# Kernel tuning notes

Measured on AMD Instinct MI355X. Metric: run time of the kernel, lower is better.

Reference implementation:

```python
import jax, jax.numpy as jnp
import numpy as np

INNER_DIM = 64
HEAD_NUM = 8
D_MODEL = 512

def setup_inputs() -> dict:
    key = jax.random.key(0)
    k1, k2, k3 = jax.random.split(key, 3)
    x = jax.random.normal(k1, (4, 2048, D_MODEL), dtype=jnp.float32)
    # Keras 'uniform' initializer: U(-0.05, 0.05)
    kernel = jax.random.uniform(k2, (3 * HEAD_NUM, D_MODEL, INNER_DIM), dtype=jnp.float32, minval=-0.05, maxval=0.05)
    head_kernel = jax.random.uniform(k3, (INNER_DIM * HEAD_NUM, D_MODEL), dtype=jnp.float32, minval=-0.05, maxval=0.05)
    return {"x": x, "kernel": kernel, "head_kernel": head_kernel}

def reference(x, kernel, head_kernel):
    H, K = HEAD_NUM, INNER_DIM
    # kernel is interleaved per head: [Q0,K0,V0, Q1,K1,V1, ...]
    w = kernel.reshape(H, 3, kernel.shape[1], K)  # (H, 3, D, K)
    wq, wk, wv = w[:, 0], w[:, 1], w[:, 2]        # each (H, D, K)
    q = jnp.einsum('bsd,hdk->bhsk', x, wq)
    k = jnp.einsum('bsd,hdk->bhsk', x, wk)
    v = jnp.einsum('bsd,hdk->bhsk', x, wv)
    scores = jnp.einsum('bhsk,bhtk->bhst', q, k) / jnp.sqrt(jnp.asarray(K, x.dtype))
    probs = jax.nn.softmax(scores, axis=-1)
    o = jnp.einsum('bhst,bhtk->bhsk', probs, v)   # (B, H, S, K)
    B, _, S, _ = o.shape
    # concat over heads along last dim matches (B, S, H*K) with head-major order
    concated = jnp.transpose(o, (0, 2, 1, 3)).reshape(B, S, H * K)
    return jnp.einsum('bse,ed->bsd', concated, head_kernel)
```

## Files before the change

kernel.cpp:

```cpp
#include <hip/hip_runtime.h>
#include <math.h>

#define D_MODEL 512
#define INNER 64
#define HEADS 8
#define BATCH 4
#define SEQ 2048
#define BHN (BATCH*HEADS)
#define PER_MAT ((size_t)BHN*SEQ*INNER)

typedef __attribute__((ext_vector_type(8))) short short8;
typedef __attribute__((ext_vector_type(4))) float floatx4;

#if __has_builtin(__builtin_amdgcn_exp2f)
#define EXP2F(x) __builtin_amdgcn_exp2f(x)
#else
#define EXP2F(x) exp2f(x)
#endif

__device__ __forceinline__ void split_bf(float f, unsigned short& h, unsigned short& l) {
    unsigned int u = __float_as_uint(f);
    h = (unsigned short)(u >> 16);
    float hf = __uint_as_float(u & 0xffff0000u);
    l = (unsigned short)(__float_as_uint(f - hf) >> 16);
}

__device__ __forceinline__ void split4(const float* f, uint2& ph, uint2& pl) {
    unsigned int h[4], l[4];
#pragma unroll
    for (int j = 0; j < 4; ++j) {
        unsigned short hu, lu;
        split_bf(f[j], hu, lu);
        h[j] = hu; l[j] = lu;
    }
    ph.x = h[0] | (h[1] << 16); ph.y = h[2] | (h[3] << 16);
    pl.x = l[0] | (l[1] << 16); pl.y = l[2] | (l[3] << 16);
}

__global__ __launch_bounds__(256) void split_x(const float* __restrict__ X,
                                               unsigned short* __restrict__ Xh,
                                               unsigned short* __restrict__ Xl) {
    size_t base = ((size_t)blockIdx.x * 256 + threadIdx.x) * 8;
    float4 a = *(const float4*)&X[base];
    float4 b = *(const float4*)&X[base + 4];
    uint2 h0, l0, h1, l1;
    split4((const float*)&a, h0, l0);
    split4((const float*)&b, h1, l1);
    *(uint4*)&Xh[base] = make_uint4(h0.x, h0.y, h1.x, h1.y);
    *(uint4*)&Xl[base] = make_uint4(l0.x, l0.y, l1.x, l1.y);
}

__global__ __launch_bounds__(256) void split_w(const float* __restrict__ kern,
                                               unsigned short* __restrict__ Wth,
                                               unsigned short* __restrict__ Wtl) {
    __shared__ float tile[64 * 65];
    const int t = threadIdx.x;
    const int mat = blockIdx.x, k0 = blockIdx.y * 64;
#pragma unroll
    for (int c = 0; c < 4; ++c) {
        int idx = t + c * 256;
        int kl = idx >> 4, i4 = idx & 15;
        float4 v = *(const float4*)&kern[((size_t)mat * 512 + k0 + kl) * 64 + i4 * 4];
        tile[(i4 * 4 + 0) * 65 + kl] = v.x;
        tile[(i4 * 4 + 1) * 65 + kl] = v.y;
        tile[(i4 * 4 + 2) * 65 + kl] = v.z;
        tile[(i4 * 4 + 3) * 65 + kl] = v.w;
    }
    __syncthreads();
    {
        int i = t >> 2, kq = t & 3;
        uint2 h0, l0, h1, l1, h2, l2, h3, l3;
        float f[16];
#pragma unroll
        for (int jj = 0; jj < 16; ++jj) f[jj] = tile[i * 65 + kq * 16 + jj];
        split4(f, h0, l0); split4(f + 4, h1, l1);
        split4(f + 8, h2, l2); split4(f + 12, h3, l3);
        size_t off = ((size_t)mat * 64 + i) * 512 + k0 + kq * 16;
        *(uint4*)&Wth[off]     = make_uint4(h0.x, h0.y, h1.x, h1.y);
        *(uint4*)&Wth[off + 8] = make_uint4(h2.x, h2.y, h3.x, h3.y);
        *(uint4*)&Wtl[off]     = make_uint4(l0.x, l0.y, l1.x, l1.y);
        *(uint4*)&Wtl[off + 8] = make_uint4(l2.x, l2.y, l3.x, l3.y);
    }
}

__global__ __launch_bounds__(256) void split_hk(const float* __restrict__ HK,
                                                unsigned short* __restrict__ Hth,
                                                unsigned short* __restrict__ Htl) {
    __shared__ float tile[64 * 65];
    const int t = threadIdx.x;
    const int n0 = blockIdx.x * 64, k0 = blockIdx.y * 64;
#pragma unroll
    for (int c = 0; c < 4; ++c) {
        int idx = t + c * 256;
        int kl = idx >> 4, n4 = idx & 15;
        float4 v = *(const float4*)&HK[(size_t)(k0 + kl) * 512 + n0 + n4 * 4];
        tile[(n4 * 4 + 0) * 65 + kl] = v.x;
        tile[(n4 * 4 + 1) * 65 + kl] = v.y;
        tile[(n4 * 4 + 2) * 65 + kl] = v.z;
        tile[(n4 * 4 + 3) * 65 + kl] = v.w;
    }
    __syncthreads();
    {
        int i = t >> 2, kq = t & 3;
        uint2 h0, l0, h1, l1, h2, l2, h3, l3;
        float f[16];
#pragma unroll
        for (int jj = 0; jj < 16; ++jj) f[jj] = tile[i * 65 + kq * 16 + jj];
        split4(f, h0, l0); split4(f + 4, h1, l1);
        split4(f + 8, h2, l2); split4(f + 12, h3, l3);
        size_t off = (size_t)(n0 + i) * 512 + k0 + kq * 16;
        *(uint4*)&Hth[off]     = make_uint4(h0.x, h0.y, h1.x, h1.y);
        *(uint4*)&Hth[off + 8] = make_uint4(h2.x, h2.y, h3.x, h3.y);
        *(uint4*)&Htl[off]     = make_uint4(l0.x, l0.y, l1.x, l1.y);
        *(uint4*)&Htl[off + 8] = make_uint4(l2.x, l2.y, l3.x, l3.y);
    }
}

__global__ __launch_bounds__(256) __attribute__((amdgpu_waves_per_eu(2, 2)))
void qkv_mfma(const unsigned short* __restrict__ Xh,
              const unsigned short* __restrict__ Xl,
              const unsigned short* __restrict__ Wth,
              const unsigned short* __restrict__ Wtl,
              unsigned short* __restrict__ Qh,
              unsigned short* __restrict__ Ql,
              unsigned short* __restrict__ Kh,
              unsigned short* __restrict__ Kl,
              unsigned short* __restrict__ Vth,
              unsigned short* __restrict__ Vtl) {
    __shared__ __align__(16) unsigned short smem[16384];
    unsigned short* Ah = smem;
    unsigned short* Al = smem + 4096;
    unsigned short* Bh = smem + 8192;
    unsigned short* Bl = smem + 12288;

    const int t = threadIdx.x;
    const int w = t >> 6, lane = t & 63;
    const int quad = lane >> 4, l16 = lane & 15;
    const int wm = w & 1, wn = w >> 1;
    const int r0 = blockIdx.x * 128, n0 = blockIdx.y * 128;

    floatx4 acc[4][4];
#pragma unroll
    for (int mt = 0; mt < 4; ++mt)
#pragma unroll
        for (int nt = 0; nt < 4; ++nt) acc[mt][nt] = (floatx4)(0.f);

    for (int ko = 0; ko < 16; ++ko) {
        const int k0 = ko * 32;
        __syncthreads();
#pragma unroll
        for (int c = 0; c < 2; ++c) {
            int idx = t + c * 256;
            int row = idx >> 2, part = idx & 3;
            size_t src = (size_t)(r0 + row) * 512 + k0 + part * 8;
            *(uint4*)&Ah[row * 32 + part * 8] = *(const uint4*)&Xh[src];
            *(uint4*)&Al[row * 32 + part * 8] = *(const uint4*)&Xl[src];
        }
#pragma unroll
        for (int c = 0; c < 2; ++c) {
            int idx = t + c * 256;
            int n = idx >> 2, part = idx & 3;
            size_t src = (size_t)(n0 + n) * 512 + k0 + part * 8;
            *(uint4*)&Bh[n * 32 + part * 8] = *(const uint4*)&Wth[src];
            *(uint4*)&Bl[n * 32 + part * 8] = *(const uint4*)&Wtl[src];
        }
        __syncthreads();

        short8 af[4], alf[4], bf[4], blf[4];
#pragma unroll
        for (int mt = 0; mt < 4; ++mt) {
            af[mt]  = *(const short8*)&Ah[(wm * 64 + mt * 16 + l16) * 32 + quad * 8];
            alf[mt] = *(const short8*)&Al[(wm * 64 + mt * 16 + l16) * 32 + quad * 8];
        }
#pragma unroll
        for (int nt = 0; nt < 4; ++nt) {
            bf[nt]  = *(const short8*)&Bh[(wn * 64 + nt * 16 + l16) * 32 + quad * 8];
            blf[nt] = *(const short8*)&Bl[(wn * 64 + nt * 16 + l16) * 32 + quad * 8];
        }
#pragma unroll
        for (int mt = 0; mt < 4; ++mt)
#pragma unroll
            for (int nt = 0; nt < 4; ++nt) {
                acc[mt][nt] = __builtin_amdgcn_mfma_f32_16x16x32_bf16(af[mt], bf[nt], acc[mt][nt], 0, 0, 0);
                acc[mt][nt] = __builtin_amdgcn_mfma_f32_16x16x32_bf16(af[mt], blf[nt], acc[mt][nt], 0, 0, 0);
                acc[mt][nt] = __builtin_amdgcn_mfma_f32_16x16x32_bf16(alf[mt], bf[nt], acc[mt][nt], 0, 0, 0);
            }
    }

    __syncthreads();
    const int mat = (n0 + wn * 64) >> 6;
    const int h = mat / 3, j = mat - 3 * h;
    const size_t bh = (size_t)(r0 >> 11) * HEADS + h;
    float* pw = (float*)smem + w * 1088;
    const float scale = (j == 0) ? 0.18033688011112042f : 1.0f;

#pragma unroll
    for (int mt = 0; mt < 4; ++mt) {
        asm volatile("" ::: "memory");
#pragma unroll
        for (int nt = 0; nt < 4; ++nt)
#pragma unroll
            for (int r = 0; r < 4; ++r)
                pw[(quad * 4 + r) * 68 + nt * 16 + l16] = acc[mt][nt][r] * scale;
        asm volatile("s_waitcnt lgkmcnt(0)" ::: "memory");
        const int sbase = (r0 & 2047) + wm * 64 + mt * 16;
        if (j < 2) {
            unsigned short* dh = (j == 0) ? Qh : Kh;
            unsigned short* dl = (j == 0) ? Ql : Kl;
            float f[16];
            const float* pr = pw + l16 * 68 + quad * 16;
#pragma unroll
            for (int jj = 0; jj < 16; ++jj) f[jj] = pr[jj];
            uint2 h0, l0, h1, l1, h2, l2, h3, l3;
            split4(f, h0, l0); split4(f + 4, h1, l1);
            split4(f + 8, h2, l2); split4(f + 12, h3, l3);
            size_t off = (bh * SEQ + sbase + l16) * 64 + quad * 16;
            *(uint4*)&dh[off]     = make_uint4(h0.x, h0.y, h1.x, h1.y);
            *(uint4*)&dh[off + 8] = make_uint4(h2.x, h2.y, h3.x, h3.y);
            *(uint4*)&dl[off]     = make_uint4(l0.x, l0.y, l1.x, l1.y);
            *(uint4*)&dl[off + 8] = make_uint4(l2.x, l2.y, l3.x, l3.y);
        } else {
            float f[16];
#pragma unroll
            for (int ss = 0; ss < 16; ++ss) f[ss] = pw[ss * 68 + lane];
            uint2 h0, l0, h1, l1, h2, l2, h3, l3;
            split4(f, h0, l0); split4(f + 4, h1, l1);
            split4(f + 8, h2, l2); split4(f + 12, h3, l3);
            size_t bb = (bh * 64 + lane) * SEQ + (size_t)(sbase & ~31);
            const int a4 = (sbase & 16) ? 4 : 0;
            *(uint2*)&Vth[bb + a4]      = h0;
            *(uint2*)&Vth[bb + 8 + a4]  = h1;
            *(uint2*)&Vth[bb + 16 + a4] = h2;
            *(uint2*)&Vth[bb + 24 + a4] = h3;
            *(uint2*)&Vtl[bb + a4]      = l0;
            *(uint2*)&Vtl[bb + 8 + a4]  = l1;
            *(uint2*)&Vtl[bb + 16 + a4] = l2;
            *(uint2*)&Vtl[bb + 24 + a4] = l3;
        }
    }
}

__global__ __launch_bounds__(256) __attribute__((amdgpu_waves_per_eu(2, 2)))
void attn_mfma(
        const unsigned short* __restrict__ Qh_g, const unsigned short* __restrict__ Ql_g,
        const unsigned short* __restrict__ Kh_g, const unsigned short* __restrict__ Kl_g,
        const unsigned short* __restrict__ Vth_g, const unsigned short* __restrict__ Vtl_g,
        unsigned short* __restrict__ Oh_g, unsigned short* __restrict__ Ol_g) {
    __shared__ __align__(16) unsigned short smem[4 * 4608];
    unsigned short* Ksh = smem;
    unsigned short* Ksl = smem + 4608;
    unsigned short* Vsh = smem + 2 * 4608;
    unsigned short* Vsl = smem + 3 * 4608;

    const int t = threadIdx.x;
    const int w = t >> 6, lane = t & 63;
    const int quad = lane >> 4, l16 = lane & 15;
    const int bh = blockIdx.x;
    const int qbase = blockIdx.y * 128 + w * 32;

    short8 qhf[2][2], qlf[2][2];
#pragma unroll
    for (int qg = 0; qg < 2; ++qg) {
        const unsigned short* p = Qh_g + ((size_t)bh * SEQ + qbase + qg * 16 + l16) * INNER + quad * 8;
        qhf[qg][0] = *(const short8*)p;
        qhf[qg][1] = *(const short8*)(p + 32);
        const unsigned short* p2 = Ql_g + ((size_t)bh * SEQ + qbase + qg * 16 + l16) * INNER + quad * 8;
        qlf[qg][0] = *(const short8*)p2;
        qlf[qg][1] = *(const short8*)(p2 + 32);
    }

    floatx4 o[2][4];
#pragma unroll
    for (int qg = 0; qg < 2; ++qg)
#pragma unroll
        for (int nt = 0; nt < 4; ++nt) o[qg][nt] = (floatx4)(0.f);
    float mrun[2] = {-1e30f, -1e30f};
    float lrun[2] = {0.f, 0.f};

    const uint4* ksrc_h = (const uint4*)(Kh_g + (size_t)bh * SEQ * INNER);
    const uint4* ksrc_l = (const uint4*)(Kl_g + (size_t)bh * SEQ * INNER);
    const uint4* vsrc_h = (const uint4*)(Vth_g + (size_t)bh * INNER * SEQ);
    const uint4* vsrc_l = (const uint4*)(Vtl_g + (size_t)bh * INNER * SEQ);

    uint4 pkh[2], pkl[2], pvh[2], pvl[2];
#pragma unroll
    for (int ii = 0; ii < 2; ++ii) {
        int id = t + ii * 256, row = id >> 3, part = id & 7;
        pkh[ii] = ksrc_h[id];
        pkl[ii] = ksrc_l[id];
        pvh[ii] = vsrc_h[row * 256 + part];
        pvl[ii] = vsrc_l[row * 256 + part];
    }

    for (int kt = 0; kt < 32; ++kt) {
        __syncthreads();
#pragma unroll
        for (int ii = 0; ii < 2; ++ii) {
            int id = t + ii * 256, row = id >> 3, part = id & 7;
            int dst = row * 72 + part * 8;
            *(uint4*)&Ksh[dst] = pkh[ii];
            *(uint4*)&Ksl[dst] = pkl[ii];
            *(uint4*)&Vsh[dst] = pvh[ii];
            *(uint4*)&Vsl[dst] = pvl[ii];
        }
        __syncthreads();

        floatx4 s[2][4];
        __builtin_amdgcn_s_setprio(1);
#pragma unroll
        for (int st = 0; st < 4; ++st) {
            const unsigned short* ka = &Ksh[(st * 16 + l16) * 72 + quad * 8];
            const unsigned short* kb = &Ksl[(st * 16 + l16) * 72 + quad * 8];
            short8 kh0 = *(const short8*)ka;
            short8 kh1 = *(const short8*)(ka + 32);
            short8 kl0 = *(const short8*)kb;
            short8 kl1 = *(const short8*)(kb + 32);
#pragma unroll
            for (int qg = 0; qg < 2; ++qg) {
                floatx4 a = (floatx4)(0.f);
                a = __builtin_amdgcn_mfma_f32_16x16x32_bf16(kh0, qhf[qg][0], a, 0, 0, 0);
                a = __builtin_amdgcn_mfma_f32_16x16x32_bf16(kh1, qhf[qg][1], a, 0, 0, 0);
                a = __builtin_amdgcn_mfma_f32_16x16x32_bf16(kl0, qhf[qg][0], a, 0, 0, 0);
                a = __builtin_amdgcn_mfma_f32_16x16x32_bf16(kl1, qhf[qg][1], a, 0, 0, 0);
                a = __builtin_amdgcn_mfma_f32_16x16x32_bf16(kh0, qlf[qg][0], a, 0, 0, 0);
                a = __builtin_amdgcn_mfma_f32_16x16x32_bf16(kh1, qlf[qg][1], a, 0, 0, 0);
                s[qg][st] = a;
            }
        }
        __builtin_amdgcn_s_setprio(0);

        if (kt + 1 < 32) {
#pragma unroll
            for (int ii = 0; ii < 2; ++ii) {
                int id = t + ii * 256, row = id >> 3, part = id & 7;
                pkh[ii] = ksrc_h[(kt + 1) * 512 + id];
                pkl[ii] = ksrc_l[(kt + 1) * 512 + id];
                pvh[ii] = vsrc_h[row * 256 + (kt + 1) * 8 + part];
                pvl[ii] = vsrc_l[row * 256 + (kt + 1) * 8 + part];
            }
        }

#pragma unroll
        for (int qg = 0; qg < 2; ++qg) {
            float mloc = s[qg][0][0];
#pragma unroll
            for (int st = 0; st < 4; ++st)
#pragma unroll
                for (int r = 0; r < 4; ++r) mloc = fmaxf(mloc, s[qg][st][r]);
            mloc = fmaxf(mloc, __shfl_xor(mloc, 16));
            mloc = fmaxf(mloc, __shfl_xor(mloc, 32));
            if (!__all(mloc - mrun[qg] <= 8.f)) {
                float mn = fmaxf(mrun[qg], mloc);
                float alpha = EXP2F(mrun[qg] - mn);
                mrun[qg] = mn;
                lrun[qg] *= alpha;
#pragma unroll
                for (int nt = 0; nt < 4; ++nt) o[qg][nt] = o[qg][nt] * alpha;
            }
            float rs = 0.f;
#pragma unroll
            for (int st = 0; st < 4; ++st)
#pragma unroll
                for (int r = 0; r < 4; ++r) {
                    float p = EXP2F(s[qg][st][r] - mrun[qg]);
                    s[qg][st][r] = p;
                    rs += p;
                }
            rs += __shfl_xor(rs, 16);
            rs += __shfl_xor(rs, 32);
            lrun[qg] += rs;
        }

#pragma unroll
        for (int half = 0; half < 2; ++half) {
            short8 phf[2], plf[2];
#pragma unroll
            for (int qg = 0; qg < 2; ++qg)
#pragma unroll
                for (int j = 0; j < 8; ++j) {
                    unsigned short hu, lu;
                    split_bf(s[qg][2 * half + (j >> 2)][j & 3], hu, lu);
                    phf[qg][j] = (short)hu;
                    plf[qg][j] = (short)lu;
                }
            __builtin_amdgcn_s_setprio(1);
#pragma unroll
            for (int nt = 0; nt < 4; ++nt) {
                const unsigned short* va = &Vsh[(nt * 16 + l16) * 72 + half * 32 + quad * 8];
                const unsigned short* vb = &Vsl[(nt * 16 + l16) * 72 + half * 32 + quad * 8];
                short8 vh = *(const short8*)va;
                short8 vl = *(const short8*)vb;
#pragma unroll
                for (int qg = 0; qg < 2; ++qg) {
                    o[qg][nt] = __builtin_amdgcn_mfma_f32_16x16x32_bf16(vh, phf[qg], o[qg][nt], 0, 0, 0);
                    o[qg][nt] = __builtin_amdgcn_mfma_f32_16x16x32_bf16(vh, plf[qg], o[qg][nt], 0, 0, 0);
                    o[qg][nt] = __builtin_amdgcn_mfma_f32_16x16x32_bf16(vl, phf[qg], o[qg][nt], 0, 0, 0);
                }
            }
            __builtin_amdgcn_s_setprio(0);
        }
    }

    __syncthreads();
#pragma unroll
    for (int qg = 0; qg < 2; ++qg) {
        const float inv = 1.f / lrun[qg];
        float* pq = (float*)smem + (2 * w + qg) * 1088;
#pragma unroll
        for (int nt = 0; nt < 4; ++nt) {
            float4 v = make_float4(o[qg][nt][0] * inv, o[qg][nt][1] * inv,
                                   o[qg][nt][2] * inv, o[qg][nt][3] * inv);
            *(float4*)&pq[l16 * 68 + nt * 16 + quad * 4] = v;
        }
    }
    asm volatile("s_waitcnt lgkmcnt(0)" ::: "memory");
#pragma unroll
    for (int qg = 0; qg < 2; ++qg) {
        const float* pq = (const float*)smem + (2 * w + qg) * 1088 + l16 * 68 + quad * 16;
        float f[16];
#pragma unroll
        for (int jj = 0; jj < 16; ++jj) f[jj] = pq[jj];
        uint2 h0, l0, h1, l1, h2, l2, h3, l3;
        split4(f, h0, l0); split4(f + 4, h1, l1);
        split4(f + 8, h2, l2); split4(f + 12, h3, l3);
        size_t off = ((size_t)bh * SEQ + qbase + qg * 16 + l16) * 64 + quad * 16;
        *(uint4*)&Oh_g[off]     = make_uint4(h0.x, h0.y, h1.x, h1.y);
        *(uint4*)&Oh_g[off + 8] = make_uint4(h2.x, h2.y, h3.x, h3.y);
        *(uint4*)&Ol_g[off]     = make_uint4(l0.x, l0.y, l1.x, l1.y);
        *(uint4*)&Ol_g[off + 8] = make_uint4(l2.x, l2.y, l3.x, l3.y);
    }
}

__global__ __launch_bounds__(256) void out_proj_mfma(const unsigned short* __restrict__ Oh,
                                                     const unsigned short* __restrict__ Ol,
                                                     const unsigned short* __restrict__ Hth,
                                                     const unsigned short* __restrict__ Htl,
                                                     float* __restrict__ Y) {
    __shared__ __align__(16) unsigned short smem[12288];
    unsigned short* Ah = smem;
    unsigned short* Al = smem + 2048;
    unsigned short* Bh = smem + 4096;
    unsigned short* Bl = smem + 8192;

    const int t = threadIdx.x;
    const int w = t >> 6, lane = t & 63;
    const int quad = lane >> 4, l16 = lane & 15;
    const int wm = w & 1, wn = w >> 1;
    const int r0 = blockIdx.x * 64, n0 = blockIdx.y * 128;
    const int b = r0 >> 11;

    floatx4 acc[2][4];
#pragma unroll
    for (int mt = 0; mt < 2; ++mt)
#pragma unroll
        for (int nt = 0; nt < 4; ++nt) acc[mt][nt] = (floatx4)(0.f);

    for (int ko = 0; ko < 16; ++ko) {
        const int h = ko >> 1, d0 = (ko & 1) * 32;
        const size_t bh = (size_t)b * HEADS + h;
        const int k0 = ko * 32;
        __syncthreads();
        {
            int row = t >> 2, part = t & 3;
            size_t src = (bh * SEQ + (r0 & 2047) + row) * 64 + d0 + part * 8;
            *(uint4*)&Ah[row * 32 + part * 8] = *(const uint4*)&Oh[src];
            *(uint4*)&Al[row * 32 + part * 8] = *(const uint4*)&Ol[src];
        }
#pragma unroll
        for (int c = 0; c < 2; ++c) {
            int idx = t + c * 256;
            int n = idx >> 2, part = idx & 3;
            size_t src = (size_t)(n0 + n) * 512 + k0 + part * 8;
            *(uint4*)&Bh[n * 32 + part * 8] = *(const uint4*)&Hth[src];
            *(uint4*)&Bl[n * 32 + part * 8] = *(const uint4*)&Htl[src];
        }
        __syncthreads();

        short8 af[2], alf[2], bf[4], blf[4];
#pragma unroll
        for (int mt = 0; mt < 2; ++mt) {
            af[mt]  = *(const short8*)&Ah[(wm * 32 + mt * 16 + l16) * 32 + quad * 8];
            alf[mt] = *(const short8*)&Al[(wm * 32 + mt * 16 + l16) * 32 + quad * 8];
        }
#pragma unroll
        for (int nt = 0; nt < 4; ++nt) {
            bf[nt]  = *(const short8*)&Bh[(wn * 64 + nt * 16 + l16) * 32 + quad * 8];
            blf[nt] = *(const short8*)&Bl[(wn * 64 + nt * 16 + l16) * 32 + quad * 8];
        }
#pragma unroll
        for (int mt = 0; mt < 2; ++mt)
#pragma unroll
            for (int nt = 0; nt < 4; ++nt) {
                acc[mt][nt] = __builtin_amdgcn_mfma_f32_16x16x32_bf16(af[mt], bf[nt], acc[mt][nt], 0, 0, 0);
                acc[mt][nt] = __builtin_amdgcn_mfma_f32_16x16x32_bf16(af[mt], blf[nt], acc[mt][nt], 0, 0, 0);
                acc[mt][nt] = __builtin_amdgcn_mfma_f32_16x16x32_bf16(alf[mt], bf[nt], acc[mt][nt], 0, 0, 0);
            }
    }

#pragma unroll
    for (int mt = 0; mt < 2; ++mt)
#pragma unroll
        for (int nt = 0; nt < 4; ++nt)
#pragma unroll
            for (int r = 0; r < 4; ++r)
                Y[(size_t)(r0 + wm * 32 + mt * 16 + quad * 4 + r) * 512 +
                  n0 + wn * 64 + nt * 16 + l16] = acc[mt][nt][r];
}

extern "C" void kernel_launch(void* const* d_in, const int* in_sizes, int n_in,
                              void* d_out, int out_size, void* d_ws, size_t ws_size,
                              hipStream_t stream) {
    const float* x    = (const float*)d_in[0];
    const float* kern = (const float*)d_in[1];
    const float* hk   = (const float*)d_in[2];
    float* y = (float*)d_out;

    unsigned short* Qh  = (unsigned short*)d_ws;
    unsigned short* Ql  = Qh + PER_MAT;
    unsigned short* Kh  = Qh + 2 * PER_MAT;
    unsigned short* Kl  = Qh + 3 * PER_MAT;
    unsigned short* Vth = Qh + 4 * PER_MAT;
    unsigned short* Vtl = Qh + 5 * PER_MAT;
    unsigned short* Oh  = Qh + 6 * PER_MAT;
    unsigned short* Ol  = Qh + 7 * PER_MAT;
    unsigned short* Xh  = Oh;
    unsigned short* Xl  = Ol;
    unsigned short* Wth = Qh + 8 * PER_MAT;
    unsigned short* Wtl = Wth + (size_t)1536 * 512;
    unsigned short* Hth = Wtl + (size_t)1536 * 512;
    unsigned short* Htl = Hth + (size_t)512 * 512;

    split_x<<<dim3(2048), 256, 0, stream>>>(x, Xh, Xl);
    split_w<<<dim3(24, 8), 256, 0, stream>>>(kern, Wth, Wtl);
    split_hk<<<dim3(8, 8), 256, 0, stream>>>(hk, Hth, Htl);
    qkv_mfma<<<dim3(64, 12), 256, 0, stream>>>(Xh, Xl, Wth, Wtl, Qh, Ql, Kh, Kl, Vth, Vtl);
    attn_mfma<<<dim3(32, 16), 256, 0, stream>>>(Qh, Ql, Kh, Kl, Vth, Vtl, Oh, Ol);
    out_proj_mfma<<<dim3(128, 4), 256, 0, stream>>>(Oh, Ol, Hth, Htl, y);
}
```

Before: 289.3 us.

## Double-buffer K/V tiles in LDS to drop one barrier per iteration

```diff
diff --git a/kernel.cpp b/kernel.cpp
--- a/kernel.cpp
+++ b/kernel.cpp
@@ -246,11 +246,7 @@
         const unsigned short* __restrict__ Kh_g, const unsigned short* __restrict__ Kl_g,
         const unsigned short* __restrict__ Vth_g, const unsigned short* __restrict__ Vtl_g,
         unsigned short* __restrict__ Oh_g, unsigned short* __restrict__ Ol_g) {
-    __shared__ __align__(16) unsigned short smem[4 * 4608];
-    unsigned short* Ksh = smem;
-    unsigned short* Ksl = smem + 4608;
-    unsigned short* Vsh = smem + 2 * 4608;
-    unsigned short* Vsl = smem + 3 * 4608;
+    __shared__ __align__(16) unsigned short smem[2 * 4 * 4608];
 
     const int t = threadIdx.x;
     const int w = t >> 6, lane = t & 63;
@@ -282,28 +278,51 @@
     const uint4* vsrc_h = (const uint4*)(Vth_g + (size_t)bh * INNER * SEQ);
     const uint4* vsrc_l = (const uint4*)(Vtl_g + (size_t)bh * INNER * SEQ);
 
+    const int sid0 = t, sid1 = t + 256;
+    const int srow0 = sid0 >> 3, spart0 = sid0 & 7;
+    const int srow1 = sid1 >> 3, spart1 = sid1 & 7;
+    const int sdst0 = srow0 * 72 + spart0 * 8;
+    const int sdst1 = srow1 * 72 + spart1 * 8;
+
     uint4 pkh[2], pkl[2], pvh[2], pvl[2];
-#pragma unroll
-    for (int ii = 0; ii < 2; ++ii) {
-        int id = t + ii * 256, row = id >> 3, part = id & 7;
-        pkh[ii] = ksrc_h[id];
-        pkl[ii] = ksrc_l[id];
-        pvh[ii] = vsrc_h[row * 256 + part];
-        pvl[ii] = vsrc_l[row * 256 + part];
-    }
+
+#define LOADT(kt_) do {                                                      \
+        pkh[0] = ksrc_h[(kt_) * 512 + sid0];                                 \
+        pkl[0] = ksrc_l[(kt_) * 512 + sid0];                                 \
+        pvh[0] = vsrc_h[srow0 * 256 + (kt_) * 8 + spart0];                   \
+        pvl[0] = vsrc_l[srow0 * 256 + (kt_) * 8 + spart0];                   \
+        pkh[1] = ksrc_h[(kt_) * 512 + sid1];                                 \
+        pkl[1] = ksrc_l[(kt_) * 512 + sid1];                                 \
+        pvh[1] = vsrc_h[srow1 * 256 + (kt_) * 8 + spart1];                   \
+        pvl[1] = vsrc_l[srow1 * 256 + (kt_) * 8 + spart1];                   \
+    } while (0)
+
+#define WRITET(base_) do {                                                   \
+        unsigned short* Kh_ = (base_);                                       \
+        unsigned short* Kl_ = (base_) + 4608;                                \
+        unsigned short* Vh_ = (base_) + 9216;                                \
+        unsigned short* Vl_ = (base_) + 13824;                               \
+        *(uint4*)&Kh_[sdst0] = pkh[0];  *(uint4*)&Kl_[sdst0] = pkl[0];       \
+        *(uint4*)&Vh_[sdst0] = pvh[0];  *(uint4*)&Vl_[sdst0] = pvl[0];       \
+        *(uint4*)&Kh_[sdst1] = pkh[1];  *(uint4*)&Kl_[sdst1] = pkl[1];       \
+        *(uint4*)&Vh_[sdst1] = pvh[1];  *(uint4*)&Vl_[sdst1] = pvl[1];       \
+    } while (0)
+
+    LOADT(0);
+    WRITET(smem);
+    LOADT(1);
+    __syncthreads();
 
     for (int kt = 0; kt < 32; ++kt) {
-        __syncthreads();
-#pragma unroll
-        for (int ii = 0; ii < 2; ++ii) {
-            int id = t + ii * 256, row = id >> 3, part = id & 7;
-            int dst = row * 72 + part * 8;
-            *(uint4*)&Ksh[dst] = pkh[ii];
-            *(uint4*)&Ksl[dst] = pkl[ii];
-            *(uint4*)&Vsh[dst] = pvh[ii];
-            *(uint4*)&Vsl[dst] = pvl[ii];
-        }
-        __syncthreads();
+        unsigned short* cbase = smem + (kt & 1) * 18432;
+        unsigned short* nbase = smem + ((kt + 1) & 1) * 18432;
+        const unsigned short* Ksh = cbase;
+        const unsigned short* Ksl = cbase + 4608;
+        const unsigned short* Vsh = cbase + 9216;
+        const unsigned short* Vsl = cbase + 13824;
+
+        if (kt + 1 < 32) WRITET(nbase);
+        if (kt + 2 < 32) LOADT(kt + 2);
 
         floatx4 s[2][4];
         __builtin_amdgcn_s_setprio(1);
@@ -329,17 +348,6 @@
         }
         __builtin_amdgcn_s_setprio(0);
 
-        if (kt + 1 < 32) {
-#pragma unroll
-            for (int ii = 0; ii < 2; ++ii) {
-                int id = t + ii * 256, row = id >> 3, part = id & 7;
-                pkh[ii] = ksrc_h[(kt + 1) * 512 + id];
-                pkl[ii] = ksrc_l[(kt + 1) * 512 + id];
-                pvh[ii] = vsrc_h[row * 256 + (kt + 1) * 8 + part];
-                pvl[ii] = vsrc_l[row * 256 + (kt + 1) * 8 + part];
-            }
-        }
-
 #pragma unroll
         for (int qg = 0; qg < 2; ++qg) {
             float mloc = s[qg][0][0];
@@ -399,9 +407,13 @@
             }
             __builtin_amdgcn_s_setprio(0);
         }
-    }
-
-    __syncthreads();
+
+        __syncthreads();
+    }
+
+#undef LOADT
+#undef WRITET
+
 #pragma unroll
     for (int qg = 0; qg < 2; ++qg) {
         const float inv = 1.f / lrun[qg];
```

Result: slower. 302.0 us (+4.4%).
